# Optimization experiments

Hardware: AMD Instinct MI355X
Metric: run time of the kernel (lower is better)

## Reference

```python
import jax, jax.numpy as jnp
import numpy as np

EPS = 1e-8  # torch CosineSimilarity default eps


def setup_inputs() -> dict:
    key = jax.random.key(0)
    ks = jax.random.split(key, 7)
    B, C, W, E, D = 64, 256, 256, 2048, 2048
    return {
        "x_img_dense": jax.random.normal(ks[0], (B, C, E), dtype=jnp.float32),
        "x_txt_dense": jax.random.normal(ks[1], (B, W, E), dtype=jnp.float32),
        "y_what_card_leader_choose": jax.random.normal(ks[2], (B, C), dtype=jnp.float32),
        "W_img1": jax.random.normal(ks[3], (D, E), dtype=jnp.float32) * 0.02,
        "b_img1": jax.random.normal(ks[4], (D,), dtype=jnp.float32) * 0.02,
        "W_words1": jax.random.normal(ks[5], (D, E), dtype=jnp.float32) * 0.02,
        "b_words1": jax.random.normal(ks[6], (D,), dtype=jnp.float32) * 0.02,
    }


def reference(x_img_dense, x_txt_dense, y_what_card_leader_choose,
              W_img1, b_img1, W_words1, b_words1):
    # Default path: img_layer=True, words_layer=True, comb_layer=False,
    # same_img_words_layer=False, gumbel=False, inference=False.
    xi = jnp.einsum('bce,de->bcd', x_img_dense, W_img1) + b_img1   # [B, C, D]
    xt = jnp.einsum('bwe,de->bwd', x_txt_dense, W_words1) + b_words1  # [B, W, D]

    # gather leader card embedding per batch element
    idx = jnp.argmax(y_what_card_leader_choose, axis=1)            # [B]
    leader = jnp.take_along_axis(xi, idx[:, None, None], axis=1)[:, 0, :]  # [B, D]

    # cosine similarity (dim=2 in torch): leader broadcast over words axis
    dot = jnp.einsum('bd,bwd->bw', leader, xt)                     # [B, W]
    denom = jnp.linalg.norm(leader, axis=-1, keepdims=True) * jnp.linalg.norm(xt, axis=-1)
    logits = dot / jnp.maximum(denom, EPS)                         # [B, W]

    # module returns softmax of `logits` (logits_final is dead code)
    return jax.nn.softmax(logits, axis=1)
```

## Files before the change

### kernel.cpp

```cpp
#include <hip/hip_runtime.h>
#include <hip/hip_bf16.h>
#include <stdint.h>

typedef unsigned short u16;
typedef __bf16 bf16x8 __attribute__((ext_vector_type(8)));
typedef float  f32x4  __attribute__((ext_vector_type(4)));
typedef float  fvec4  __attribute__((ext_vector_type(4)));

constexpr int NB = 64;
constexpr int NC = 256;
constexpr int NW = 256;
constexpr int NE = 2048;
constexpr int ND = 2048;
constexpr int MROWS = NB * NW;

constexpr int BM = 128, BN = 128, BK = 64;
constexpr int KSPLIT = 8;
constexpr int KSLICE = NE / KSPLIT;
constexpr int NSLOT = 32;

constexpr size_t OFF_LN     = 0;
constexpr size_t OFF_LDR    = 256;
constexpr size_t OFF_A0     = 524544;
constexpr size_t OFF_SHARED = 1048832;
constexpr size_t OFF_WW     = 5243136;
constexpr size_t OFF_XT     = 13631744;
constexpr size_t NEED_FULL  = OFF_XT + 67108864ull;

__device__ __forceinline__ u16 f2bf(float f) {
    uint32_t u = __float_as_uint(f);
    u += 0x7fffu + ((u >> 16) & 1u);
    return (u16)(u >> 16);
}

__global__ void k_gather(const float* __restrict__ y, const float* __restrict__ ximg,
                         u16* __restrict__ A0) {
    int r = blockIdx.x;
    int t = threadIdx.x;
    u16* dst = A0 + (size_t)r * NE;
    if (r >= NB) {
        for (int e = t; e < NE; e += 256) dst[e] = 0;
        return;
    }
    __shared__ float sv[4];
    __shared__ int   si[4];
    __shared__ int   sidx;
    float v = y[r * NC + t];
    int   i = t;
    for (int off = 1; off < 64; off <<= 1) {
        float ov = __shfl_xor(v, off, 64);
        int   oi = __shfl_xor(i, off, 64);
        if (ov > v || (ov == v && oi < i)) { v = ov; i = oi; }
    }
    if ((t & 63) == 0) { sv[t >> 6] = v; si[t >> 6] = i; }
    __syncthreads();
    if (t == 0) {
        float bv = sv[0]; int bi = si[0];
        for (int w = 1; w < 4; ++w)
            if (sv[w] > bv || (sv[w] == bv && si[w] < bi)) { bv = sv[w]; bi = si[w]; }
        sidx = bi;
    }
    __syncthreads();
    const float* src = ximg + ((size_t)r * NC + sidx) * NE;
    for (int e = t; e < NE; e += 256) dst[e] = f2bf(src[e]);
}

__global__ void k_convert2(const float* __restrict__ a, u16* __restrict__ da, int n4a,
                           const float* __restrict__ b, u16* __restrict__ db, int n4b) {
    int stride = gridDim.x * blockDim.x;
    int n4 = n4a + n4b;
    for (int i = blockIdx.x * blockDim.x + threadIdx.x; i < n4; i += stride) {
        const fvec4* sp; ushort4* dp; int j;
        if (i < n4a) { sp = (const fvec4*)a; dp = (ushort4*)da; j = i; }
        else         { sp = (const fvec4*)b; dp = (ushort4*)db; j = i - n4a; }
        fvec4 v = __builtin_nontemporal_load(&sp[j]);
        ushort4 o = { f2bf(v.x), f2bf(v.y), f2bf(v.z), f2bf(v.w) };
        dp[j] = o;
    }
}

__global__ __launch_bounds__(256) void k_gemm0(
    const u16* __restrict__ A0, const float* __restrict__ Wimg,
    float* __restrict__ part)
{
    __shared__ __align__(16) u16 sA[BM * BK];
    __shared__ __align__(16) u16 sB[BN * BK];

    const int t  = threadIdx.x;
    const int l  = t & 63;
    const int wv = t >> 6;
    const int wm = wv >> 1, wn = wv & 1;

    const int nt = blockIdx.x >> 3, ks = blockIdx.x & 7;
    const int n0 = nt * BN;
    const int kbase = ks * KSLICE;

    f32x4 acc[4][4];
    #pragma unroll
    for (int i = 0; i < 4; ++i)
        #pragma unroll
        for (int j = 0; j < 4; ++j) acc[i][j] = (f32x4){0.f, 0.f, 0.f, 0.f};

    const int lr = l >> 3, lp = l & 7;

    for (int k0 = kbase; k0 < kbase + KSLICE; k0 += BK) {
        __syncthreads();
        #pragma unroll
        for (int i = 0; i < 4; ++i) {
            int r = wv * 32 + i * 8 + lr;
            int g = lp ^ (r & 7);
            const u16* src = A0 + (size_t)r * NE + k0 + g * 8;
            __builtin_amdgcn_global_load_lds(
                (const __attribute__((address_space(1))) void*)src,
                (__attribute__((address_space(3))) void*)&sA[(wv * 32 + i * 8) * BK],
                16, 0, 0);
        }
        #pragma unroll
        for (int i = 0; i < 4; ++i) {
            int r = wv * 32 + i * 8 + lr;
            int g = lp ^ (r & 7);
            const float* src = Wimg + (size_t)(n0 + r) * NE + k0 + g * 8;
            float4 v0 = *(const float4*)src;
            float4 v1 = *(const float4*)(src + 4);
            uint4 ov;
            ov.x = (uint32_t)f2bf(v0.x) | ((uint32_t)f2bf(v0.y) << 16);
            ov.y = (uint32_t)f2bf(v0.z) | ((uint32_t)f2bf(v0.w) << 16);
            ov.z = (uint32_t)f2bf(v1.x) | ((uint32_t)f2bf(v1.y) << 16);
            ov.w = (uint32_t)f2bf(v1.z) | ((uint32_t)f2bf(v1.w) << 16);
            *(uint4*)&sB[r * BK + lp * 8] = ov;
        }
        __syncthreads();

        #pragma unroll
        for (int kk = 0; kk < 2; ++kk) {
            bf16x8 af[4], bfr[4];
            #pragma unroll
            for (int mi = 0; mi < 4; ++mi) {
                int ra = wm * 64 + mi * 16 + (l & 15);
                int g  = kk * 4 + (l >> 4);
                int p  = g ^ (ra & 7);
                af[mi] = *(const bf16x8*)&sA[ra * BK + p * 8];
            }
            #pragma unroll
            for (int nj = 0; nj < 4; ++nj) {
                int rb = wn * 64 + nj * 16 + (l & 15);
                int g  = kk * 4 + (l >> 4);
                int p  = g ^ (rb & 7);
                bfr[nj] = *(const bf16x8*)&sB[rb * BK + p * 8];
            }
            #pragma unroll
            for (int mi = 0; mi < 4; ++mi)
                #pragma unroll
                for (int nj = 0; nj < 4; ++nj)
                    acc[mi][nj] = __builtin_amdgcn_mfma_f32_16x16x32_bf16(
                        af[mi], bfr[nj], acc[mi][nj], 0, 0, 0);
        }
    }

    if (wm == 0) {
        const int quad = l >> 4, lc = l & 15;
        #pragma unroll
        for (int mi = 0; mi < 4; ++mi)
            #pragma unroll
            for (int r = 0; r < 4; ++r) {
                int m = mi * 16 + quad * 4 + r;
                #pragma unroll
                for (int nj = 0; nj < 4; ++nj) {
                    int n = n0 + wn * 64 + nj * 16 + lc;
                    part[((size_t)ks * NB + m) * ND + n] = acc[mi][nj][r];
                }
            }
    }
}

__global__ void k_leaderfix(const float* __restrict__ part, const float* __restrict__ bias,
                            float* __restrict__ leader, float* __restrict__ ln2) {
    int b = blockIdx.x, t = threadIdx.x;
    float s2 = 0.f;
    #pragma unroll
    for (int i = 0; i < 8; ++i) {
        int d = i * 256 + t;
        float s = bias[d];
        #pragma unroll
        for (int ks = 0; ks < KSPLIT; ++ks)
            s += part[((size_t)ks * NB + b) * ND + d];
        leader[(size_t)b * ND + d] = s;
        s2 += s * s;
    }
    for (int off = 1; off < 64; off <<= 1) s2 += __shfl_xor(s2, off, 64);
    __shared__ float red[4];
    if ((t & 63) == 0) red[t >> 6] = s2;
    __syncthreads();
    if (t == 0) ln2[b] = red[0] + red[1] + red[2] + red[3];
}

template<bool ABF, bool BBF>
__global__ __launch_bounds__(256) void k_gemm1(
    const void* __restrict__ Av, const void* __restrict__ Bv,
    const float* __restrict__ bias, const float* __restrict__ leader,
    float* __restrict__ dotp, float* __restrict__ ssqp)
{
    __shared__ __align__(16) u16 sA[BM * BK];
    __shared__ __align__(16) u16 sB[BN * BK];

    const int t  = threadIdx.x;
    const int l  = t & 63;
    const int wv = t >> 6;
    const int wm = wv >> 1, wn = wv & 1;

    const int mt = blockIdx.x >> 4;
    const int nt = blockIdx.x & 15;
    const int m0 = mt * BM, n0 = nt * BN;

    f32x4 acc[4][4];
    #pragma unroll
    for (int i = 0; i < 4; ++i)
        #pragma unroll
        for (int jj = 0; jj < 4; ++jj) acc[i][jj] = (f32x4){0.f, 0.f, 0.f, 0.f};

    const int lr = l >> 3, lp = l & 7;

    for (int k0 = 0; k0 < NE; k0 += BK) {
        __syncthreads();
        #pragma unroll
        for (int i = 0; i < 4; ++i) {
            int r = wv * 32 + i * 8 + lr;
            int g = lp ^ (r & 7);
            if (ABF) {
                const u16* src = (const u16*)Av + (size_t)(m0 + r) * NE + k0 + g * 8;
                __builtin_amdgcn_global_load_lds(
                    (const __attribute__((address_space(1))) void*)src,
                    (__attribute__((address_space(3))) void*)&sA[(wv * 32 + i * 8) * BK],
                    16, 0, 0);
            } else {
                const float* src = (const float*)Av + (size_t)(m0 + r) * NE + k0 + g * 8;
                float4 v0 = *(const float4*)src;
                float4 v1 = *(const float4*)(src + 4);
                uint4 ov;
                ov.x = (uint32_t)f2bf(v0.x) | ((uint32_t)f2bf(v0.y) << 16);
                ov.y = (uint32_t)f2bf(v0.z) | ((uint32_t)f2bf(v0.w) << 16);
                ov.z = (uint32_t)f2bf(v1.x) | ((uint32_t)f2bf(v1.y) << 16);
                ov.w = (uint32_t)f2bf(v1.z) | ((uint32_t)f2bf(v1.w) << 16);
                *(uint4*)&sA[r * BK + lp * 8] = ov;
            }
        }
        #pragma unroll
        for (int i = 0; i < 4; ++i) {
            int r = wv * 32 + i * 8 + lr;
            int g = lp ^ (r & 7);
            if (BBF) {
                const u16* src = (const u16*)Bv + (size_t)(n0 + r) * NE + k0 + g * 8;
                __builtin_amdgcn_global_load_lds(
                    (const __attribute__((address_space(1))) void*)src,
                    (__attribute__((address_space(3))) void*)&sB[(wv * 32 + i * 8) * BK],
                    16, 0, 0);
            } else {
                const float* src = (const float*)Bv + (size_t)(n0 + r) * NE + k0 + g * 8;
                float4 v0 = *(const float4*)src;
                float4 v1 = *(const float4*)(src + 4);
                uint4 ov;
                ov.x = (uint32_t)f2bf(v0.x) | ((uint32_t)f2bf(v0.y) << 16);
                ov.y = (uint32_t)f2bf(v0.z) | ((uint32_t)f2bf(v0.w) << 16);
                ov.z = (uint32_t)f2bf(v1.x) | ((uint32_t)f2bf(v1.y) << 16);
                ov.w = (uint32_t)f2bf(v1.z) | ((uint32_t)f2bf(v1.w) << 16);
                *(uint4*)&sB[r * BK + lp * 8] = ov;
            }
        }
        __syncthreads();

        #pragma unroll
        for (int kk = 0; kk < 2; ++kk) {
            bf16x8 af[4], bfr[4];
            #pragma unroll
            for (int mi = 0; mi < 4; ++mi) {
                int ra = wm * 64 + mi * 16 + (l & 15);
                int g  = kk * 4 + (l >> 4);
                int p  = g ^ (ra & 7);
                af[mi] = *(const bf16x8*)&sA[ra * BK + p * 8];
            }
            #pragma unroll
            for (int nj = 0; nj < 4; ++nj) {
                int rb = wn * 64 + nj * 16 + (l & 15);
                int g  = kk * 4 + (l >> 4);
                int p  = g ^ (rb & 7);
                bfr[nj] = *(const bf16x8*)&sB[rb * BK + p * 8];
            }
            #pragma unroll
            for (int mi = 0; mi < 4; ++mi)
                #pragma unroll
                for (int nj = 0; nj < 4; ++nj)
                    acc[mi][nj] = __builtin_amdgcn_mfma_f32_16x16x32_bf16(
                        af[mi], bfr[nj], acc[mi][nj], 0, 0, 0);
        }
    }

    const int quad = l >> 4, lc = l & 15;
    const int bidx = m0 >> 8;
    const int slot = nt * 2 + wn;
    float bia[4], ldr[4];
    #pragma unroll
    for (int nj = 0; nj < 4; ++nj) {
        int n = n0 + wn * 64 + nj * 16 + lc;
        bia[nj] = bias[n];
        ldr[nj] = leader[(size_t)bidx * ND + n];
    }
    #pragma unroll
    for (int mi = 0; mi < 4; ++mi) {
        #pragma unroll
        for (int r = 0; r < 4; ++r) {
            int m = m0 + wm * 64 + mi * 16 + quad * 4 + r;
            float pd = 0.f, ps = 0.f;
            #pragma unroll
            for (int nj = 0; nj < 4; ++nj) {
                float v = acc[mi][nj][r] + bia[nj];
                pd += ldr[nj] * v;
                ps += v * v;
            }
            for (int off = 1; off <= 8; off <<= 1) {
                pd += __shfl_xor(pd, off, 64);
                ps += __shfl_xor(ps, off, 64);
            }
            if (lc == 0) {
                dotp[(size_t)slot * MROWS + m] = pd;
                ssqp[(size_t)slot * MROWS + m] = ps;
            }
        }
    }
}

__global__ void k_final(const float* __restrict__ dotp, const float* __restrict__ ssqp,
                        const float* __restrict__ ln2, float* __restrict__ out) {
    int b = blockIdx.x, w = threadIdx.x;
    __shared__ float redm[4], reds[4];
    int m = b * NW + w;
    float dt = 0.f, sq = 0.f;
    #pragma unroll
    for (int s = 0; s < NSLOT; ++s) {
        dt += dotp[(size_t)s * MROWS + m];
        sq += ssqp[(size_t)s * MROWS + m];
    }
    float dn = sqrtf(ln2[b]) * sqrtf(sq);
    float lg = dt / fmaxf(dn, 1e-8f);
    float mx = lg;
    for (int off = 1; off < 64; off <<= 1) mx = fmaxf(mx, __shfl_xor(mx, off, 64));
    int wvi = w >> 6;
    if ((w & 63) == 0) redm[wvi] = mx;
    __syncthreads();
    mx = fmaxf(fmaxf(redm[0], redm[1]), fmaxf(redm[2], redm[3]));
    float e = __expf(lg - mx);
    float s = e;
    for (int off = 1; off < 64; off <<= 1) s += __shfl_xor(s, off, 64);
    if ((w & 63) == 0) reds[wvi] = s;
    __syncthreads();
    s = reds[0] + reds[1] + reds[2] + reds[3];
    out[b * NW + w] = e / s;
}

extern "C" void kernel_launch(void* const* d_in, const int* in_sizes, int n_in,
                              void* d_out, int out_size, void* d_ws, size_t ws_size,
                              hipStream_t stream) {
    const float* ximg = (const float*)d_in[0];
    const float* xtxt = (const float*)d_in[1];
    const float* y    = (const float*)d_in[2];
    const float* Wimg = (const float*)d_in[3];
    const float* bimg = (const float*)d_in[4];
    const float* Wwrd = (const float*)d_in[5];
    const float* bwrd = (const float*)d_in[6];
    float* out = (float*)d_out;

    char* ws = (char*)d_ws;
    float* ln2  = (float*)(ws + OFF_LN);
    float* ldr  = (float*)(ws + OFF_LDR);
    u16*   A0   = (u16*)(ws + OFF_A0);
    float* part = (float*)(ws + OFF_SHARED);
    float* dotp = (float*)(ws + OFF_SHARED);
    float* ssqp = (float*)(ws + OFF_SHARED + (size_t)NSLOT * MROWS * 4);
    u16*   WWb  = (u16*)(ws + OFF_WW);
    u16*   XTb  = (u16*)(ws + OFF_XT);

    const bool preconv = ws_size >= NEED_FULL;

    k_gather<<<BM, 256, 0, stream>>>(y, ximg, A0);
    k_gemm0<<<(ND / BN) * KSPLIT, 256, 0, stream>>>(A0, Wimg, part);
    k_leaderfix<<<NB, 256, 0, stream>>>(part, bimg, ldr, ln2);

    if (preconv) {
        k_convert2<<<4096, 256, 0, stream>>>(Wwrd, WWb, ND * NE / 4,
                                             xtxt, XTb, MROWS * NE / 4);
        k_gemm1<true, true><<<(MROWS / BM) * (ND / BN), 256, 0, stream>>>(
            XTb, WWb, bwrd, ldr, dotp, ssqp);
    } else {
        k_gemm1<false, false><<<(MROWS / BM) * (ND / BN), 256, 0, stream>>>(
            xtxt, Wwrd, bwrd, ldr, dotp, ssqp);
    }
    k_final<<<NB, 256, 0, stream>>>(dotp, ssqp, ln2, out);
}
```

Before: 464.0 us.

## Fuse gather, leader reduction and argmax into neighbouring kernels to cut launches

Folds the argmax into the conversion kernel as an extra block, and has gemm0 read the selected image rows directly and convert them to bf16, removing the separate gather kernel. The leader-fix kernel is gone: gemm1 and the final kernel each recompute the leader from the split-K partials, and the K-split count is halved. gemm1 also combines its two N-waves through shared memory, which halves the dot and sum-of-squares slots the final kernel must read. Together these cut the launch count and intermediate traffic, in exchange for redundant leader recomputation in every gemm1 block and less parallelism in gemm0.

```diff
diff --git a/kernel.cpp b/kernel.cpp
--- a/kernel.cpp
+++ b/kernel.cpp
@@ -15,17 +15,17 @@
 constexpr int MROWS = NB * NW;
 
 constexpr int BM = 128, BN = 128, BK = 64;
-constexpr int KSPLIT = 8;
+constexpr int KSPLIT = 4;
 constexpr int KSLICE = NE / KSPLIT;
-constexpr int NSLOT = 32;
-
-constexpr size_t OFF_LN     = 0;
-constexpr size_t OFF_LDR    = 256;
-constexpr size_t OFF_A0     = 524544;
-constexpr size_t OFF_SHARED = 1048832;
-constexpr size_t OFF_WW     = 5243136;
-constexpr size_t OFF_XT     = 13631744;
-constexpr size_t NEED_FULL  = OFF_XT + 67108864ull;
+constexpr int NSLOT = 16;
+
+constexpr size_t OFF_IDX  = 0;
+constexpr size_t OFF_PART = 256;
+constexpr size_t OFF_DOTP = 2097408;
+constexpr size_t OFF_SSQP = 3145984;
+constexpr size_t OFF_WW   = 4194560;
+constexpr size_t OFF_XT   = 12583168;
+constexpr size_t NEED_FULL = OFF_XT + 67108864ull;
 
 __device__ __forceinline__ u16 f2bf(float f) {
     uint32_t u = __float_as_uint(f);
@@ -33,43 +33,31 @@
     return (u16)(u >> 16);
 }
 
-__global__ void k_gather(const float* __restrict__ y, const float* __restrict__ ximg,
-                         u16* __restrict__ A0) {
-    int r = blockIdx.x;
-    int t = threadIdx.x;
-    u16* dst = A0 + (size_t)r * NE;
-    if (r >= NB) {
-        for (int e = t; e < NE; e += 256) dst[e] = 0;
+__global__ void k_conv_argmax(const float* __restrict__ a, u16* __restrict__ da, int n4a,
+                              const float* __restrict__ b, u16* __restrict__ db, int n4b,
+                              const float* __restrict__ y, int* __restrict__ idx) {
+    if (blockIdx.x == 0) {
+        int t = threadIdx.x;
+        int row = t >> 2, c = t & 3;
+        float best = -3.4e38f; int bi = 0;
+        for (int k = 0; k < 64; ++k) {
+            int j = c + k * 4;
+            float v = y[row * NC + j];
+            if (v > best) { best = v; bi = j; }
+        }
+        #pragma unroll
+        for (int off = 1; off <= 2; off <<= 1) {
+            float ov = __shfl_xor(best, off, 64);
+            int   oi = __shfl_xor(bi,   off, 64);
+            if (ov > best || (ov == best && oi < bi)) { best = ov; bi = oi; }
+        }
+        if (c == 0) idx[row] = bi;
         return;
     }
-    __shared__ float sv[4];
-    __shared__ int   si[4];
-    __shared__ int   sidx;
-    float v = y[r * NC + t];
-    int   i = t;
-    for (int off = 1; off < 64; off <<= 1) {
-        float ov = __shfl_xor(v, off, 64);
-        int   oi = __shfl_xor(i, off, 64);
-        if (ov > v || (ov == v && oi < i)) { v = ov; i = oi; }
-    }
-    if ((t & 63) == 0) { sv[t >> 6] = v; si[t >> 6] = i; }
-    __syncthreads();
-    if (t == 0) {
-        float bv = sv[0]; int bi = si[0];
-        for (int w = 1; w < 4; ++w)
-            if (sv[w] > bv || (sv[w] == bv && si[w] < bi)) { bv = sv[w]; bi = si[w]; }
-        sidx = bi;
-    }
-    __syncthreads();
-    const float* src = ximg + ((size_t)r * NC + sidx) * NE;
-    for (int e = t; e < NE; e += 256) dst[e] = f2bf(src[e]);
-}
-
-__global__ void k_convert2(const float* __restrict__ a, u16* __restrict__ da, int n4a,
-                           const float* __restrict__ b, u16* __restrict__ db, int n4b) {
-    int stride = gridDim.x * blockDim.x;
+    int i0 = (blockIdx.x - 1) * blockDim.x + threadIdx.x;
+    int stride = (gridDim.x - 1) * blockDim.x;
     int n4 = n4a + n4b;
-    for (int i = blockIdx.x * blockDim.x + threadIdx.x; i < n4; i += stride) {
+    for (int i = i0; i < n4; i += stride) {
         const fvec4* sp; ushort4* dp; int j;
         if (i < n4a) { sp = (const fvec4*)a; dp = (ushort4*)da; j = i; }
         else         { sp = (const fvec4*)b; dp = (ushort4*)db; j = i - n4a; }
@@ -80,20 +68,23 @@
 }
 
 __global__ __launch_bounds__(256) void k_gemm0(
-    const u16* __restrict__ A0, const float* __restrict__ Wimg,
-    float* __restrict__ part)
+    const float* __restrict__ ximg, const int* __restrict__ idx,
+    const float* __restrict__ Wimg, float* __restrict__ part)
 {
     __shared__ __align__(16) u16 sA[BM * BK];
     __shared__ __align__(16) u16 sB[BN * BK];
+    __shared__ int s_idx[64];
 
     const int t  = threadIdx.x;
     const int l  = t & 63;
     const int wv = t >> 6;
     const int wm = wv >> 1, wn = wv & 1;
 
-    const int nt = blockIdx.x >> 3, ks = blockIdx.x & 7;
+    const int nt = blockIdx.x >> 2, ks = blockIdx.x & 3;
     const int n0 = nt * BN;
     const int kbase = ks * KSLICE;
+
+    if (t < 64) s_idx[t] = idx[t];
 
     f32x4 acc[4][4];
     #pragma unroll
@@ -109,17 +100,26 @@
         for (int i = 0; i < 4; ++i) {
             int r = wv * 32 + i * 8 + lr;
             int g = lp ^ (r & 7);
-            const u16* src = A0 + (size_t)r * NE + k0 + g * 8;
-            __builtin_amdgcn_global_load_lds(
-                (const __attribute__((address_space(1))) void*)src,
-                (__attribute__((address_space(3))) void*)&sA[(wv * 32 + i * 8) * BK],
-                16, 0, 0);
+            if (r < 64) {
+                const float* src = ximg + ((size_t)r * NC + s_idx[r]) * NE + k0 + g * 8;
+                float4 v0 = *(const float4*)src;
+                float4 v1 = *(const float4*)(src + 4);
+                uint4 ov;
+                ov.x = (uint32_t)f2bf(v0.x) | ((uint32_t)f2bf(v0.y) << 16);
+                ov.y = (uint32_t)f2bf(v0.z) | ((uint32_t)f2bf(v0.w) << 16);
+                ov.z = (uint32_t)f2bf(v1.x) | ((uint32_t)f2bf(v1.y) << 16);
+                ov.w = (uint32_t)f2bf(v1.z) | ((uint32_t)f2bf(v1.w) << 16);
+                *(uint4*)&sA[r * BK + lp * 8] = ov;
+            } else {
+                *(uint4*)&sA[r * BK + lp * 8] = (uint4){0, 0, 0, 0};
+            }
         }
         #pragma unroll
         for (int i = 0; i < 4; ++i) {
             int r = wv * 32 + i * 8 + lr;
             int g = lp ^ (r & 7);
-            const float* src = Wimg + (size_t)(n0 + r) * NE + k0 + g * 8;
+            const float* src = Wimg + (size_t)(n0 + r) * NE + kbase + (k0 - kbase) + g * 8;
+            src = Wimg + (size_t)(n0 + r) * NE + k0 + g * 8;
             float4 v0 = *(const float4*)src;
             float4 v1 = *(const float4*)(src + 4);
             uint4 ov;
@@ -173,31 +173,11 @@
     }
 }
 
-__global__ void k_leaderfix(const float* __restrict__ part, const float* __restrict__ bias,
-                            float* __restrict__ leader, float* __restrict__ ln2) {
-    int b = blockIdx.x, t = threadIdx.x;
-    float s2 = 0.f;
-    #pragma unroll
-    for (int i = 0; i < 8; ++i) {
-        int d = i * 256 + t;
-        float s = bias[d];
-        #pragma unroll
-        for (int ks = 0; ks < KSPLIT; ++ks)
-            s += part[((size_t)ks * NB + b) * ND + d];
-        leader[(size_t)b * ND + d] = s;
-        s2 += s * s;
-    }
-    for (int off = 1; off < 64; off <<= 1) s2 += __shfl_xor(s2, off, 64);
-    __shared__ float red[4];
-    if ((t & 63) == 0) red[t >> 6] = s2;
-    __syncthreads();
-    if (t == 0) ln2[b] = red[0] + red[1] + red[2] + red[3];
-}
-
 template<bool ABF, bool BBF>
 __global__ __launch_bounds__(256) void k_gemm1(
     const void* __restrict__ Av, const void* __restrict__ Bv,
-    const float* __restrict__ bias, const float* __restrict__ leader,
+    const float* __restrict__ bwrd, const float* __restrict__ bimg,
+    const float* __restrict__ part,
     float* __restrict__ dotp, float* __restrict__ ssqp)
 {
     __shared__ __align__(16) u16 sA[BM * BK];
@@ -296,19 +276,23 @@
 
     const int quad = l >> 4, lc = l & 15;
     const int bidx = m0 >> 8;
-    const int slot = nt * 2 + wn;
     float bia[4], ldr[4];
     #pragma unroll
     for (int nj = 0; nj < 4; ++nj) {
         int n = n0 + wn * 64 + nj * 16 + lc;
-        bia[nj] = bias[n];
-        ldr[nj] = leader[(size_t)bidx * ND + n];
-    }
+        bia[nj] = bwrd[n];
+        float ld = bimg[n];
+        #pragma unroll
+        for (int ks = 0; ks < KSPLIT; ++ks)
+            ld += part[((size_t)ks * NB + bidx) * ND + n];
+        ldr[nj] = ld;
+    }
+    __syncthreads();
+    float* sRed = (float*)sA;
     #pragma unroll
     for (int mi = 0; mi < 4; ++mi) {
         #pragma unroll
         for (int r = 0; r < 4; ++r) {
-            int m = m0 + wm * 64 + mi * 16 + quad * 4 + r;
             float pd = 0.f, ps = 0.f;
             #pragma unroll
             for (int nj = 0; nj < 4; ++nj) {
@@ -316,44 +300,71 @@
                 pd += ldr[nj] * v;
                 ps += v * v;
             }
+            #pragma unroll
             for (int off = 1; off <= 8; off <<= 1) {
                 pd += __shfl_xor(pd, off, 64);
                 ps += __shfl_xor(ps, off, 64);
             }
             if (lc == 0) {
-                dotp[(size_t)slot * MROWS + m] = pd;
-                ssqp[(size_t)slot * MROWS + m] = ps;
-            }
-        }
-    }
-}
-
-__global__ void k_final(const float* __restrict__ dotp, const float* __restrict__ ssqp,
-                        const float* __restrict__ ln2, float* __restrict__ out) {
-    int b = blockIdx.x, w = threadIdx.x;
-    __shared__ float redm[4], reds[4];
-    int m = b * NW + w;
+                int lm = mi * 16 + quad * 4 + r;
+                sRed[(wm * 2 + wn) * 64 + lm]       = pd;
+                sRed[256 + (wm * 2 + wn) * 64 + lm] = ps;
+            }
+        }
+    }
+    __syncthreads();
+    if (t < 128) {
+        int wmm = t >> 6, lm = t & 63;
+        int m = m0 + wmm * 64 + lm;
+        dotp[(size_t)nt * MROWS + m] =
+            sRed[(wmm * 2 + 0) * 64 + lm] + sRed[(wmm * 2 + 1) * 64 + lm];
+        ssqp[(size_t)nt * MROWS + m] =
+            sRed[256 + (wmm * 2 + 0) * 64 + lm] + sRed[256 + (wmm * 2 + 1) * 64 + lm];
+    }
+}
+
+__global__ void k_final(const float* __restrict__ part, const float* __restrict__ bimg,
+                        const float* __restrict__ dotp, const float* __restrict__ ssqp,
+                        float* __restrict__ out) {
+    int b = blockIdx.x, t = threadIdx.x;
+    __shared__ float rsum[4], redm[4], reds[4];
+    float s2 = 0.f;
+    #pragma unroll
+    for (int i = 0; i < 8; ++i) {
+        int d = i * 256 + t;
+        float ld = bimg[d];
+        #pragma unroll
+        for (int ks = 0; ks < KSPLIT; ++ks)
+            ld += part[((size_t)ks * NB + b) * ND + d];
+        s2 += ld * ld;
+    }
+    for (int off = 1; off < 64; off <<= 1) s2 += __shfl_xor(s2, off, 64);
+    if ((t & 63) == 0) rsum[t >> 6] = s2;
+    __syncthreads();
+    float ln2 = rsum[0] + rsum[1] + rsum[2] + rsum[3];
+
+    int m = b * NW + t;
     float dt = 0.f, sq = 0.f;
     #pragma unroll
     for (int s = 0; s < NSLOT; ++s) {
         dt += dotp[(size_t)s * MROWS + m];
         sq += ssqp[(size_t)s * MROWS + m];
     }
-    float dn = sqrtf(ln2[b]) * sqrtf(sq);
+    float dn = sqrtf(ln2) * sqrtf(sq);
     float lg = dt / fmaxf(dn, 1e-8f);
     float mx = lg;
     for (int off = 1; off < 64; off <<= 1) mx = fmaxf(mx, __shfl_xor(mx, off, 64));
-    int wvi = w >> 6;
-    if ((w & 63) == 0) redm[wvi] = mx;
+    int wvi = t >> 6;
+    if ((t & 63) == 0) redm[wvi] = mx;
     __syncthreads();
     mx = fmaxf(fmaxf(redm[0], redm[1]), fmaxf(redm[2], redm[3]));
     float e = __expf(lg - mx);
     float s = e;
     for (int off = 1; off < 64; off <<= 1) s += __shfl_xor(s, off, 64);
-    if ((w & 63) == 0) reds[wvi] = s;
+    if ((t & 63) == 0) reds[wvi] = s;
     __syncthreads();
     s = reds[0] + reds[1] + reds[2] + reds[3];
-    out[b * NW + w] = e / s;
+    out[m] = e / s;
 }
 
 extern "C" void kernel_launch(void* const* d_in, const int* in_sizes, int n_in,
@@ -369,29 +380,27 @@
     float* out = (float*)d_out;
 
     char* ws = (char*)d_ws;
-    float* ln2  = (float*)(ws + OFF_LN);
-    float* ldr  = (float*)(ws + OFF_LDR);
-    u16*   A0   = (u16*)(ws + OFF_A0);
-    float* part = (float*)(ws + OFF_SHARED);
-    float* dotp = (float*)(ws + OFF_SHARED);
-    float* ssqp = (float*)(ws + OFF_SHARED + (size_t)NSLOT * MROWS * 4);
+    int*   idx  = (int*)(ws + OFF_IDX);
+    float* part = (float*)(ws + OFF_PART);
+    float* dotp = (float*)(ws + OFF_DOTP);
+    float* ssqp = (float*)(ws + OFF_SSQP);
     u16*   WWb  = (u16*)(ws + OFF_WW);
     u16*   XTb  = (u16*)(ws + OFF_XT);
 
     const bool preconv = ws_size >= NEED_FULL;
 
-    k_gather<<<BM, 256, 0, stream>>>(y, ximg, A0);
-    k_gemm0<<<(ND / BN) * KSPLIT, 256, 0, stream>>>(A0, Wimg, part);
-    k_leaderfix<<<NB, 256, 0, stream>>>(part, bimg, ldr, ln2);
-
     if (preconv) {
-        k_convert2<<<4096, 256, 0, stream>>>(Wwrd, WWb, ND * NE / 4,
-                                             xtxt, XTb, MROWS * NE / 4);
+        k_conv_argmax<<<4097, 256, 0, stream>>>(Wwrd, WWb, ND * NE / 4,
+                                                xtxt, XTb, MROWS * NE / 4, y, idx);
+        k_gemm0<<<(ND / BN) * KSPLIT, 256, 0, stream>>>(ximg, idx, Wimg, part);
         k_gemm1<true, true><<<(MROWS / BM) * (ND / BN), 256, 0, stream>>>(
-            XTb, WWb, bwrd, ldr, dotp, ssqp);
+            XTb, WWb, bwrd, bimg, part, dotp, ssqp);
     } else {
+        k_conv_argmax<<<1, 256, 0, stream>>>(nullptr, nullptr, 0,
+                                             nullptr, nullptr, 0, y, idx);
+        k_gemm0<<<(ND / BN) * KSPLIT, 256, 0, stream>>>(ximg, idx, Wimg, part);
         k_gemm1<false, false><<<(MROWS / BM) * (ND / BN), 256, 0, stream>>>(
-            xtxt, Wwrd, bwrd, ldr, dotp, ssqp);
-    }
-    k_final<<<NB, 256, 0, stream>>>(dotp, ssqp, ln2, out);
-}
+            xtxt, Wwrd, bwrd, bimg, part, dotp, ssqp);
+    }
+    k_final<<<NB, 256, 0, stream>>>(part, bimg, dotp, ssqp, out);
+}
```

Measured after the change: 456.5 us. No clear change (-1.6%).
